# Kernel tuning notes

Measured on AMD Instinct MI355X. Metric: run time of the kernel, lower is better.

Reference implementation:

```python
import jax, jax.numpy as jnp
import numpy as np

N_INIT = jnp.array([17.047, 14.099, 3.625], dtype=jnp.float32)
CA_INIT = jnp.array([16.967, 12.784, 4.338], dtype=jnp.float32)
C_INIT = jnp.array([15.685, 12.755, 5.133], dtype=jnp.float32)


def _unit(x):
    return x / (jnp.linalg.norm(x, axis=-1, keepdims=True) + 1e-8)


def _place_dihedral(a, b, c, bond_angle, bond_length, torsion):
    # a,b,c: [B,3]; bond_angle/bond_length/torsion: [B]
    ab = b - a
    bc = _unit(c - b)
    cr = jnp.cross(ab, bc)
    crn = jnp.linalg.norm(cr, axis=-1, keepdims=True)
    n_main = _unit(cr)
    # collinear fallback (per-element; almost never triggers for real angles)
    perp = jnp.zeros_like(bc).at[..., 0].set(1.0)
    ct = jnp.cross(bc, perp)
    ctn = jnp.linalg.norm(ct, axis=-1, keepdims=True)
    perp2 = jnp.where(ctn < 1e-6, jnp.zeros_like(bc).at[..., 1].set(1.0), perp)
    n_fb = _unit(jnp.cross(bc, perp2))
    n = jnp.where(crn < 1e-6, n_fb, n_main)
    nbc = jnp.cross(n, bc)
    m = jnp.stack([bc, nbc, n], axis=-1)  # [B,3,3]
    d_local = jnp.stack([
        -bond_length * jnp.cos(bond_angle),
        bond_length * jnp.cos(torsion) * jnp.sin(bond_angle),
        bond_length * jnp.sin(torsion) * jnp.sin(bond_angle),
    ], axis=-1)  # [B,3]
    d = jnp.einsum('bij,bj->bi', m, d_local)
    return d + c


def _nerf_build(phi, psi, omega, bond_lengths, bond_angles):
    B, L = phi.shape
    init = jnp.broadcast_to(jnp.stack([N_INIT, CA_INIT, C_INIT]), (B, 3, 3))
    # per-step params, leading axis = residue index i in [0, L-2]
    xs = (
        psi[:, :L - 1].T,                 # psi_i
        omega[:, :L - 1].T,               # omega_i
        phi[:, 1:].T,                     # phi_{i+1}
        bond_lengths[:, :L - 1, 2].T,     # C-N length
        bond_lengths[:, :L - 1, 0].T,     # N-CA length
        bond_lengths[:, :L - 1, 1].T,     # CA-C length
        bond_angles[:, :L - 1, 1].T,      # CA-C-N angle
        bond_angles[:, :L - 1, 2].T,      # C-N-CA angle
        bond_angles[:, :L - 1, 0].T,      # N-CA-C angle
    )

    def step(prev, x):
        psi_i, omega_i, phi_i, len_cn, len_nca, len_cac, ang_cacn, ang_cnca, ang_ncac = x
        a, b, c = prev[:, 0], prev[:, 1], prev[:, 2]
        n = _place_dihedral(a, b, c, ang_cacn, len_cn, psi_i)
        ca = _place_dihedral(b, c, n, ang_cnca, len_nca, omega_i)
        cc = _place_dihedral(c, n, ca, ang_ncac, len_cac, phi_i)
        new = jnp.stack([n, ca, cc], axis=1)  # [B,3,3]
        return new, new

    _, outs = jax.lax.scan(step, init, xs)  # [L-1,B,3,3]
    rest = outs.transpose(1, 0, 2, 3).reshape(B, 3 * (L - 1), 3)
    return jnp.concatenate([init, rest], axis=1)  # [B, 3L, 3]


def setup_inputs() -> dict:
    key = jax.random.key(0)
    k0, k1, k2, k3, k4 = jax.random.split(key, 5)
    B, L = 4096, 512
    phi = jax.random.normal(k0, (B, L), dtype=jnp.float32)
    psi = jax.random.normal(k1, (B, L), dtype=jnp.float32)
    omega = jax.random.normal(k2, (B, L), dtype=jnp.float32)
    # realistic positive bond lengths (~1.0-1.5 A) and bond angles (~1.5-2.3 rad)
    bond_lengths = 1.0 + 0.5 * jax.random.uniform(k3, (B, L, 3), dtype=jnp.float32)
    bond_angles = 1.5 + 0.8 * jax.random.uniform(k4, (B, L, 3), dtype=jnp.float32)
    return {"phi": phi, "psi": psi, "omega": omega,
            "bond_lengths": bond_lengths, "bond_angles": bond_angles}


def reference(phi, psi, omega, bond_lengths, bond_angles):
    return _nerf_build(phi, psi, omega, bond_lengths, bond_angles)
```

## Files before the change

kernel.cpp:

```cpp
#include <hip/hip_runtime.h>
#include <math.h>


#define LCH 512

struct Xf { float r[9]; float t[3]; };

__device__ __forceinline__ Xf xf_compose(const Xf& A, const Xf& B) {
  Xf C;
#pragma unroll
  for (int i = 0; i < 3; ++i) {
    float a0 = A.r[3*i+0], a1 = A.r[3*i+1], a2 = A.r[3*i+2];
    C.r[3*i+0] = a0*B.r[0] + a1*B.r[3] + a2*B.r[6];
    C.r[3*i+1] = a0*B.r[1] + a1*B.r[4] + a2*B.r[7];
    C.r[3*i+2] = a0*B.r[2] + a1*B.r[5] + a2*B.r[8];
    C.t[i]     = a0*B.t[0] + a1*B.t[1] + a2*B.t[2] + A.t[i];
  }
  return C;
}

__device__ __forceinline__ void xf_step(Xf& P, float theta, float len, float tau) {
  float st, ct, sx, cx;
  __sincosf(theta, &st, &ct);
  __sincosf(tau, &sx, &cx);
  float ux = -ct, uy = cx*st, uz = sx*st;
  float v0 = -st, v1 = -ct*cx, v2 = -ct*sx;
  float c00 = P.r[0]*ux + P.r[1]*uy + P.r[2]*uz;
  float c10 = P.r[3]*ux + P.r[4]*uy + P.r[5]*uz;
  float c20 = P.r[6]*ux + P.r[7]*uy + P.r[8]*uz;
  float c01 = P.r[0]*v0 + P.r[1]*v1 + P.r[2]*v2;
  float c11 = P.r[3]*v0 + P.r[4]*v1 + P.r[5]*v2;
  float c21 = P.r[6]*v0 + P.r[7]*v1 + P.r[8]*v2;
  float c02 = P.r[2]*cx - P.r[1]*sx;
  float c12 = P.r[5]*cx - P.r[4]*sx;
  float c22 = P.r[8]*cx - P.r[7]*sx;
  P.t[0] += len*c00; P.t[1] += len*c10; P.t[2] += len*c20;
  P.r[0]=c00; P.r[1]=c01; P.r[2]=c02;
  P.r[3]=c10; P.r[4]=c11; P.r[5]=c12;
  P.r[6]=c20; P.r[7]=c21; P.r[8]=c22;
}

__device__ __forceinline__ void xf_set_delta(Xf& P, float theta, float len, float tau) {
  float st, ct, sx, cx;
  __sincosf(theta, &st, &ct);
  __sincosf(tau, &sx, &cx);
  float ux = -ct, uy = cx*st, uz = sx*st;
  P.r[0]=ux; P.r[1]=-st;    P.r[2]=0.f;
  P.r[3]=uy; P.r[4]=-ct*cx; P.r[5]=-sx;
  P.r[6]=uz; P.r[7]=-ct*sx; P.r[8]=cx;
  P.t[0]=len*ux; P.t[1]=len*uy; P.t[2]=len*uz;
}

__device__ __forceinline__ void xf_identity(Xf& A) {
  A.r[0]=1.f; A.r[1]=0.f; A.r[2]=0.f;
  A.r[3]=0.f; A.r[4]=1.f; A.r[5]=0.f;
  A.r[6]=0.f; A.r[7]=0.f; A.r[8]=1.f;
  A.t[0]=0.f; A.t[1]=0.f; A.t[2]=0.f;
}

__device__ __forceinline__ Xf xf_shfl_up(const Xf& P, int d) {
  Xf O;
#pragma unroll
  for (int i = 0; i < 9; ++i) O.r[i] = __shfl_up(P.r[i], d, 64);
#pragma unroll
  for (int i = 0; i < 3; ++i) O.t[i] = __shfl_up(P.t[i], d, 64);
  return O;
}

__device__ __forceinline__ float rfl(float x) {
  return __int_as_float(__builtin_amdgcn_readfirstlane(__float_as_int(x)));
}

__global__ __launch_bounds__(256) void nerf_r20_kernel(
    const float* __restrict__ g_phi, const float* __restrict__ g_psi,
    const float* __restrict__ g_omg, const float* __restrict__ g_bl,
    const float* __restrict__ g_ba, float* __restrict__ g_out)
{
  __shared__ float s_tot[36];
  __shared__ float s_out[4608];

  const int t    = threadIdx.x;
  const int lane = t & 63;
  const int wave = t >> 6;
  const int chain = blockIdx.x;

  const float* phir = g_phi + (size_t)chain * LCH;
  const float* psir = g_psi + (size_t)chain * LCH;
  const float* omgr = g_omg + (size_t)chain * LCH;
  const float* blr  = g_bl  + (size_t)chain * (LCH*3);
  const float* bar  = g_ba  + (size_t)chain * (LCH*3);

  const int j2 = 2 * t;
  const int b6 = 6 * t;

  float2 ps2 = *(const float2*)(psir + j2);
  float2 om2 = *(const float2*)(omgr + j2);
  float2 ph2 = *(const float2*)(phir + j2);
  float2 lb0 = *(const float2*)(blr + b6);
  float2 lb1 = *(const float2*)(blr + b6 + 2);
  float2 lb2 = *(const float2*)(blr + b6 + 4);
  float2 ab0 = *(const float2*)(bar + b6);
  float2 ab1 = *(const float2*)(bar + b6 + 2);
  float2 ab2 = *(const float2*)(bar + b6 + 4);

  float psA  = __shfl_up(ps2.y, 1, 64);
  float omA  = __shfl_up(om2.y, 1, 64);
  float blA0 = __shfl_up(lb1.y, 1, 64);
  float blA1 = __shfl_up(lb2.x, 1, 64);
  float blA2 = __shfl_up(lb2.y, 1, 64);
  float baA0 = __shfl_up(ab1.y, 1, 64);
  float baA1 = __shfl_up(ab2.x, 1, 64);
  float baA2 = __shfl_up(ab2.y, 1, 64);
  if (lane == 0 && t != 0) {
    psA  = psir[j2 - 1];
    omA  = omgr[j2 - 1];
    blA0 = blr[b6 - 3]; blA1 = blr[b6 - 2]; blA2 = blr[b6 - 1];
    baA0 = bar[b6 - 3]; baA1 = bar[b6 - 2]; baA2 = bar[b6 - 1];
  }
  const float phA = ph2.x;
  const float psB = ps2.x, omB = om2.x, phB = ph2.y;
  const float blB0 = lb0.x, blB1 = lb0.y, blB2 = lb1.x;
  const float baB0 = ab0.x, baB1 = ab0.y, baB2 = ab1.x;

  Xf PA, PB;
  xf_set_delta(PA, baA1, blA2, psA);
  xf_set_delta(PB, baB1, blB2, psB);
  xf_step(PA, baA2, blA0, omA);
  xf_step(PB, baB2, blB0, omB);
  xf_step(PA, baA0, blA1, phA);
  xf_step(PB, baB0, blB1, phB);
  if (t == 0) xf_identity(PA);
  Xf P = xf_compose(PA, PB);

#pragma unroll
  for (int d = 1; d < 64; d <<= 1) {
    Xf O = xf_shfl_up(P, d);
    if (lane >= d) P = xf_compose(O, P);
  }

  if (lane == 63 && wave < 3) {
#pragma unroll
    for (int i = 0; i < 9; ++i) s_tot[12*wave + i] = P.r[i];
#pragma unroll
    for (int i = 0; i < 3; ++i) s_tot[12*wave + 9 + i] = P.t[i];
  }
  Xf E = xf_shfl_up(P, 1);
  __syncthreads();

  if (t == 0) {
    Xf T0, T1, T2;
#pragma unroll
    for (int i = 0; i < 9; ++i) { T0.r[i]=s_tot[i]; T1.r[i]=s_tot[12+i]; T2.r[i]=s_tot[24+i]; }
#pragma unroll
    for (int i = 0; i < 3; ++i) { T0.t[i]=s_tot[9+i]; T1.t[i]=s_tot[21+i]; T2.t[i]=s_tot[33+i]; }
    Xf C2 = xf_compose(T0, T1);
    Xf C3 = xf_compose(C2, T2);
#pragma unroll
    for (int i = 0; i < 9; ++i) { s_tot[12+i] = C2.r[i]; s_tot[24+i] = C3.r[i]; }
#pragma unroll
    for (int i = 0; i < 3; ++i) { s_tot[21+i] = C2.t[i]; s_tot[33+i] = C3.t[i]; }
  }
  __syncthreads();

  Xf A;
  A.r[0]=-0.849699f; A.r[1]=-0.223843f; A.r[2]=-0.477398f;
  A.r[3]=-0.019221f; A.r[4]= 0.917962f; A.r[5]=-0.396206f;
  A.r[6]= 0.526919f; A.r[7]=-0.327477f; A.r[8]=-0.784291f;
  A.t[0]=15.685f; A.t[1]=12.755f; A.t[2]=5.133f;
  if (wave >= 1) {
    const int o = 12 * (wave - 1);
    Xf T;
#pragma unroll
    for (int i = 0; i < 9; ++i) T.r[i] = rfl(s_tot[o + i]);
#pragma unroll
    for (int i = 0; i < 3; ++i) T.t[i] = rfl(s_tot[o + 9 + i]);
    A = xf_compose(A, T);
  }
  if (lane > 0) A = xf_compose(A, E);

  float* o = s_out + 18 * t;
  if (t == 0) {
    o[0]=17.047f; o[1]=14.099f; o[2]=3.625f;
    o[3]=16.967f; o[4]=12.784f; o[5]=4.338f;
    o[6]=15.685f; o[7]=12.755f; o[8]=5.133f;
  } else {
    xf_step(A, baA1, blA2, psA);
    o[0]=A.t[0]; o[1]=A.t[1]; o[2]=A.t[2];
    xf_step(A, baA2, blA0, omA);
    o[3]=A.t[0]; o[4]=A.t[1]; o[5]=A.t[2];
    xf_step(A, baA0, blA1, phA);
    o[6]=A.t[0]; o[7]=A.t[1]; o[8]=A.t[2];
  }
  xf_step(A, baB1, blB2, psB);
  o[9]=A.t[0];  o[10]=A.t[1]; o[11]=A.t[2];
  xf_step(A, baB2, blB0, omB);
  o[12]=A.t[0]; o[13]=A.t[1]; o[14]=A.t[2];
  xf_step(A, baB0, blB1, phB);
  o[15]=A.t[0]; o[16]=A.t[1]; o[17]=A.t[2];
  __syncthreads();

  float* orow = g_out + (size_t)chain * 4608;
#pragma unroll
  for (int q = 0; q < 9; ++q) {
    const int g = 2*t + 512*q;
    float2 v = *(const float2*)(s_out + g);
    *(float2*)(orow + g) = v;
  }
}

extern "C" void kernel_launch(void* const* d_in, const int* in_sizes, int n_in,
                              void* d_out, int out_size, void* d_ws, size_t ws_size,
                              hipStream_t stream) {
  const float* phi = (const float*)d_in[0];
  const float* psi = (const float*)d_in[1];
  const float* omg = (const float*)d_in[2];
  const float* bl  = (const float*)d_in[3];
  const float* ba  = (const float*)d_in[4];
  float* out = (float*)d_out;
  const int B = in_sizes[0] / LCH;
  hipLaunchKernelGGL(nerf_r20_kernel, dim3(B), dim3(256), 0, stream,
                     phi, psi, omg, bl, ba, out);
}
```

Baseline: 146.2 us.

## Use one residue per thread with 512-thread blocks and 8-wave scan

```diff
diff --git a/kernel.cpp b/kernel.cpp
--- a/kernel.cpp
+++ b/kernel.cpp
@@ -67,16 +67,12 @@
   return O;
 }
 
-__device__ __forceinline__ float rfl(float x) {
-  return __int_as_float(__builtin_amdgcn_readfirstlane(__float_as_int(x)));
-}
-
-__global__ __launch_bounds__(256) void nerf_r20_kernel(
+__global__ __launch_bounds__(512) void nerf_r21_kernel(
     const float* __restrict__ g_phi, const float* __restrict__ g_psi,
     const float* __restrict__ g_omg, const float* __restrict__ g_bl,
     const float* __restrict__ g_ba, float* __restrict__ g_out)
 {
-  __shared__ float s_tot[36];
+  __shared__ float s_tot[84];
   __shared__ float s_out[4608];
 
   const int t    = threadIdx.x;
@@ -90,47 +86,32 @@
   const float* blr  = g_bl  + (size_t)chain * (LCH*3);
   const float* bar  = g_ba  + (size_t)chain * (LCH*3);
 
-  const int j2 = 2 * t;
-  const int b6 = 6 * t;
-
-  float2 ps2 = *(const float2*)(psir + j2);
-  float2 om2 = *(const float2*)(omgr + j2);
-  float2 ph2 = *(const float2*)(phir + j2);
-  float2 lb0 = *(const float2*)(blr + b6);
-  float2 lb1 = *(const float2*)(blr + b6 + 2);
-  float2 lb2 = *(const float2*)(blr + b6 + 4);
-  float2 ab0 = *(const float2*)(bar + b6);
-  float2 ab1 = *(const float2*)(bar + b6 + 2);
-  float2 ab2 = *(const float2*)(bar + b6 + 4);
-
-  float psA  = __shfl_up(ps2.y, 1, 64);
-  float omA  = __shfl_up(om2.y, 1, 64);
-  float blA0 = __shfl_up(lb1.y, 1, 64);
-  float blA1 = __shfl_up(lb2.x, 1, 64);
-  float blA2 = __shfl_up(lb2.y, 1, 64);
-  float baA0 = __shfl_up(ab1.y, 1, 64);
-  float baA1 = __shfl_up(ab2.x, 1, 64);
-  float baA2 = __shfl_up(ab2.y, 1, 64);
+  float ps  = psir[t];
+  float om  = omgr[t];
+  float ph  = phir[t];
+  float bl0 = blr[3*t], bl1 = blr[3*t+1], bl2 = blr[3*t+2];
+  float ba0 = bar[3*t], ba1 = bar[3*t+1], ba2 = bar[3*t+2];
+
+  float psA  = __shfl_up(ps, 1, 64);
+  float omA  = __shfl_up(om, 1, 64);
+  float blA0 = __shfl_up(bl0, 1, 64);
+  float blA1 = __shfl_up(bl1, 1, 64);
+  float blA2 = __shfl_up(bl2, 1, 64);
+  float baA0 = __shfl_up(ba0, 1, 64);
+  float baA1 = __shfl_up(ba1, 1, 64);
+  float baA2 = __shfl_up(ba2, 1, 64);
   if (lane == 0 && t != 0) {
-    psA  = psir[j2 - 1];
-    omA  = omgr[j2 - 1];
-    blA0 = blr[b6 - 3]; blA1 = blr[b6 - 2]; blA2 = blr[b6 - 1];
-    baA0 = bar[b6 - 3]; baA1 = bar[b6 - 2]; baA2 = bar[b6 - 1];
-  }
-  const float phA = ph2.x;
-  const float psB = ps2.x, omB = om2.x, phB = ph2.y;
-  const float blB0 = lb0.x, blB1 = lb0.y, blB2 = lb1.x;
-  const float baB0 = ab0.x, baB1 = ab0.y, baB2 = ab1.x;
-
-  Xf PA, PB;
-  xf_set_delta(PA, baA1, blA2, psA);
-  xf_set_delta(PB, baB1, blB2, psB);
-  xf_step(PA, baA2, blA0, omA);
-  xf_step(PB, baB2, blB0, omB);
-  xf_step(PA, baA0, blA1, phA);
-  xf_step(PB, baB0, blB1, phB);
-  if (t == 0) xf_identity(PA);
-  Xf P = xf_compose(PA, PB);
+    psA  = psir[t - 1];
+    omA  = omgr[t - 1];
+    blA0 = blr[3*t - 3]; blA1 = blr[3*t - 2]; blA2 = blr[3*t - 1];
+    baA0 = bar[3*t - 3]; baA1 = bar[3*t - 2]; baA2 = bar[3*t - 1];
+  }
+
+  Xf P;
+  xf_set_delta(P, baA1, blA2, psA);
+  xf_step(P, baA2, blA0, omA);
+  xf_step(P, baA0, blA1, ph);
+  if (t == 0) xf_identity(P);
 
 #pragma unroll
   for (int d = 1; d < 64; d <<= 1) {
@@ -138,7 +119,7 @@
     if (lane >= d) P = xf_compose(O, P);
   }
 
-  if (lane == 63 && wave < 3) {
+  if (lane == 63 && wave < 7) {
 #pragma unroll
     for (int i = 0; i < 9; ++i) s_tot[12*wave + i] = P.r[i];
 #pragma unroll
@@ -148,17 +129,23 @@
   __syncthreads();
 
   if (t == 0) {
-    Xf T0, T1, T2;
-#pragma unroll
-    for (int i = 0; i < 9; ++i) { T0.r[i]=s_tot[i]; T1.r[i]=s_tot[12+i]; T2.r[i]=s_tot[24+i]; }
-#pragma unroll
-    for (int i = 0; i < 3; ++i) { T0.t[i]=s_tot[9+i]; T1.t[i]=s_tot[21+i]; T2.t[i]=s_tot[33+i]; }
-    Xf C2 = xf_compose(T0, T1);
-    Xf C3 = xf_compose(C2, T2);
-#pragma unroll
-    for (int i = 0; i < 9; ++i) { s_tot[12+i] = C2.r[i]; s_tot[24+i] = C3.r[i]; }
-#pragma unroll
-    for (int i = 0; i < 3; ++i) { s_tot[21+i] = C2.t[i]; s_tot[33+i] = C3.t[i]; }
+    Xf C;
+#pragma unroll
+    for (int i = 0; i < 9; ++i) C.r[i] = s_tot[i];
+#pragma unroll
+    for (int i = 0; i < 3; ++i) C.t[i] = s_tot[9+i];
+    for (int w = 1; w < 7; ++w) {
+      Xf T;
+#pragma unroll
+      for (int i = 0; i < 9; ++i) T.r[i] = s_tot[12*w + i];
+#pragma unroll
+      for (int i = 0; i < 3; ++i) T.t[i] = s_tot[12*w + 9 + i];
+      C = xf_compose(C, T);
+#pragma unroll
+      for (int i = 0; i < 9; ++i) s_tot[12*w + i] = C.r[i];
+#pragma unroll
+      for (int i = 0; i < 3; ++i) s_tot[12*w + 9 + i] = C.t[i];
+    }
   }
   __syncthreads();
 
@@ -171,14 +158,14 @@
     const int o = 12 * (wave - 1);
     Xf T;
 #pragma unroll
-    for (int i = 0; i < 9; ++i) T.r[i] = rfl(s_tot[o + i]);
-#pragma unroll
-    for (int i = 0; i < 3; ++i) T.t[i] = rfl(s_tot[o + 9 + i]);
+    for (int i = 0; i < 9; ++i) T.r[i] = s_tot[o + i];
+#pragma unroll
+    for (int i = 0; i < 3; ++i) T.t[i] = s_tot[o + 9 + i];
     A = xf_compose(A, T);
   }
   if (lane > 0) A = xf_compose(A, E);
 
-  float* o = s_out + 18 * t;
+  float* o = s_out + 9 * t;
   if (t == 0) {
     o[0]=17.047f; o[1]=14.099f; o[2]=3.625f;
     o[3]=16.967f; o[4]=12.784f; o[5]=4.338f;
@@ -188,23 +175,16 @@
     o[0]=A.t[0]; o[1]=A.t[1]; o[2]=A.t[2];
     xf_step(A, baA2, blA0, omA);
     o[3]=A.t[0]; o[4]=A.t[1]; o[5]=A.t[2];
-    xf_step(A, baA0, blA1, phA);
+    xf_step(A, baA0, blA1, ph);
     o[6]=A.t[0]; o[7]=A.t[1]; o[8]=A.t[2];
   }
-  xf_step(A, baB1, blB2, psB);
-  o[9]=A.t[0];  o[10]=A.t[1]; o[11]=A.t[2];
-  xf_step(A, baB2, blB0, omB);
-  o[12]=A.t[0]; o[13]=A.t[1]; o[14]=A.t[2];
-  xf_step(A, baB0, blB1, phB);
-  o[15]=A.t[0]; o[16]=A.t[1]; o[17]=A.t[2];
   __syncthreads();
 
   float* orow = g_out + (size_t)chain * 4608;
 #pragma unroll
   for (int q = 0; q < 9; ++q) {
-    const int g = 2*t + 512*q;
-    float2 v = *(const float2*)(s_out + g);
-    *(float2*)(orow + g) = v;
+    const int g = t + 512*q;
+    orow[g] = s_out[g];
   }
 }
 
@@ -218,6 +198,6 @@
   const float* ba  = (const float*)d_in[4];
   float* out = (float*)d_out;
   const int B = in_sizes[0] / LCH;
-  hipLaunchKernelGGL(nerf_r20_kernel, dim3(B), dim3(256), 0, stream,
+  hipLaunchKernelGGL(nerf_r21_kernel, dim3(B), dim3(512), 0, stream,
                      phi, psi, omg, bl, ba, out);
 }
```

After: 169.7 us. 1.16x slower.
